# Kernel optimization log

Hardware: AMD Instinct MI355X
Metric: run time of the kernel (lower is better)

The kernel has to match this reference:

```python
import jax, jax.numpy as jnp
import numpy as np

M = 8192        # tokens (batch*seq)
K = 14336       # d_ff (input features of down proj)
N = 4096        # d_model (output features)
GROUP = 128     # quantization group size along K


def unpack_int4(w_packed):
    """[N, K//8] int32 -> [N, K] signed int4 values in [-8, 7] (float32)."""
    n, kp = w_packed.shape
    shifts = (jnp.arange(8, dtype=jnp.int32) * 4)  # nibble 0 = lowest bits
    nib = (w_packed[:, :, None] >> shifts) & 0xF   # [N, K//8, 8]
    nib = nib - jnp.where(nib >= 8, 16, 0)         # sign-extend 4-bit
    return nib.reshape(n, kp * 8).astype(jnp.float32)


def setup_inputs() -> dict:
    key = jax.random.key(0)
    ks = jax.random.split(key, 6)
    qx = jax.random.normal(ks[0], (M, K), dtype=jnp.float32)
    qxscale = jax.random.uniform(ks[1], (M, 1), dtype=jnp.float32) * 0.05 + 0.001
    residual = jax.random.normal(ks[2], (M, N), dtype=jnp.float32)
    weight_i4 = jax.random.randint(ks[3], (N, K // 8), jnp.iinfo(jnp.int32).min,
                                   jnp.iinfo(jnp.int32).max, dtype=jnp.int32)
    weight_scale = jax.random.uniform(ks[4], (N, K // GROUP), dtype=jnp.float32) * 0.02 + 0.001
    bias = jax.random.normal(ks[5], (N,), dtype=jnp.float32)
    return {"qx": qx, "qxscale": qxscale, "residual": residual,
            "weight_i4": weight_i4, "weight_scale": weight_scale,
            "bias": bias, "group_size": GROUP}


def reference(qx, qxscale, residual, weight_i4, weight_scale, bias, group_size):
    # 1) unpack int32 -> signed int4
    iw = unpack_int4(weight_i4)                          # [N, K]
    n, k = iw.shape
    g = k // group_size
    # 2) group-wise dequantize (one scale per group along K, per output row)
    dq = (iw.reshape(n, g, group_size) * weight_scale[:, :, None]).reshape(n, k)
    # 3) matmul x @ W^T, 4) per-token scale, residual + bias
    y = jnp.einsum('mk,nk->mn', qx, dq) * qxscale + residual + bias
    return y
```

## Files before the change

### kernel.cpp

```cpp
#include <hip/hip_runtime.h>
#include <hip/hip_bf16.h>
#include <stdint.h>

#define M_DIM 8192
#define K_DIM 14336
#define N_DIM 4096
#define GROUP_SZ 128
#define NGROUP (K_DIM / GROUP_SZ)

typedef short short8 __attribute__((ext_vector_type(8)));
typedef float f32x4 __attribute__((ext_vector_type(4)));
typedef int i32x4 __attribute__((ext_vector_type(4)));

static __device__ __forceinline__ short f2bf(float f) {
  unsigned u = __builtin_bit_cast(unsigned, f);
  u += 0x7FFFu + ((u >> 16) & 1u);
  return (short)(u >> 16);
}

static __device__ __forceinline__ void gload_lds16(const void* g, void* lds) {
  __builtin_amdgcn_global_load_lds(
      (const __attribute__((address_space(1))) unsigned int*)g,
      (__attribute__((address_space(3))) unsigned int*)lds, 16, 0, 0);
}


__global__ __launch_bounds__(256) void dp_quant_x(const float* __restrict__ x,
                                                  char* __restrict__ xq,
                                                  float* __restrict__ sx) {
  __shared__ float rowbuf[K_DIM];
  __shared__ float red[256];
  const int row = blockIdx.x;
  const int t = threadIdx.x;
  const float* xr = x + (size_t)row * K_DIM;
  float amax = 0.f;
#pragma unroll
  for (int j = 0; j < 14; ++j) {
    float4 v = *(const float4*)(xr + j * 1024 + t * 4);
    *(float4*)(rowbuf + j * 1024 + t * 4) = v;
    amax = fmaxf(amax,
                 fmaxf(fmaxf(fabsf(v.x), fabsf(v.y)), fmaxf(fabsf(v.z), fabsf(v.w))));
  }
  red[t] = amax;
  __syncthreads();
  for (int s = 128; s > 0; s >>= 1) {
    if (t < s) red[t] = fmaxf(red[t], red[t + s]);
    __syncthreads();
  }
  const float am = red[0];
  const float inv = (am > 0.f) ? 127.f / am : 0.f;
  if (t == 0) sx[row] = am * (1.f / 127.f);
  char* xo = xq + (size_t)row * K_DIM;
#pragma unroll
  for (int j = 0; j < 14; ++j) {
    float4 v = *(const float4*)(rowbuf + j * 1024 + t * 4);
    char4 q;
    q.x = (char)__float2int_rn(v.x * inv);
    q.y = (char)__float2int_rn(v.y * inv);
    q.z = (char)__float2int_rn(v.z * inv);
    q.w = (char)__float2int_rn(v.w * inv);
    *(char4*)(xo + j * 1024 + t * 4) = q;
  }
}

__global__ __launch_bounds__(256) void dp_repack_w(const int* __restrict__ wq,
                                                   const float* __restrict__ wsc,
                                                   char* __restrict__ w8,
                                                   float* __restrict__ sw) {
  __shared__ float wsl[NGROUP];
  const int n = blockIdx.x;
  const int t = threadIdx.x;
  if (t < NGROUP) wsl[t] = wsc[(size_t)n * NGROUP + t];
  __syncthreads();
  float mx = 0.f;
#pragma unroll
  for (int g = 0; g < NGROUP; ++g) mx = fmaxf(mx, wsl[g]);
  const float invsw = 15.875f / mx;
  if (t == 0) sw[n] = mx * (8.f / 127.f);
#pragma unroll
  for (int j = 0; j < 7; ++j) {
    int p = t + 256 * j;
    int w = wq[(size_t)n * (K_DIM / 8) + p];
    float sc = wsl[p >> 4] * invsw;
    unsigned lo = 0, hi = 0;
#pragma unroll
    for (int b = 0; b < 4; ++b) {
      int q = (w << (28 - 4 * b)) >> 28;
      int r = __float2int_rn((float)q * sc);
      lo |= (unsigned)(r & 0xff) << (8 * b);
    }
#pragma unroll
    for (int b = 4; b < 8; ++b) {
      int q = (w << (28 - 4 * b)) >> 28;
      int r = __float2int_rn((float)q * sc);
      hi |= (unsigned)(r & 0xff) << (8 * (b - 4));
    }
    *(uint2*)(w8 + (size_t)n * K_DIM + (size_t)p * 8) = make_uint2(lo, hi);
  }
}

__global__ __launch_bounds__(512, 2) void dp_gemm8i(
    const char* __restrict__ Xq, const char* __restrict__ Wq8,
    const float* __restrict__ sw, const float* __restrict__ sx,
    const float* __restrict__ qxscale, const float* __restrict__ residual,
    const float* __restrict__ bias, float* __restrict__ out) {
  __shared__ __align__(16) char lds[65536];

  const int tid = threadIdx.x;
  const int lane = tid & 63;
  const int wid = tid >> 6;
  const int wm = wid >> 2, wn = wid & 3;
  const int lr = lane & 15, lg = lane >> 4;

  const int wg = blockIdx.x;
  const int swz = (wg & 7) * 64 + (wg >> 3);
  const int m0 = (swz >> 4) * 256;
  const int n0 = (swz & 15) * 256;

  const int slot = (lg ^ ((lr >> 1) & 3)) << 4;
  int offA[2][4], offB[2][2];
#pragma unroll
  for (int mh = 0; mh < 2; ++mh)
#pragma unroll
    for (int mf = 0; mf < 4; ++mf)
      offA[mh][mf] = (mh * 128 + wm * 64 + mf * 16 + lr) * 64 + slot;
#pragma unroll
  for (int nh = 0; nh < 2; ++nh)
#pragma unroll
    for (int nf = 0; nf < 2; ++nf)
      offB[nh][nf] = (nh * 128 + wn * 32 + nf * 16 + lr) * 64 + slot;

  const int srow = tid >> 2;
  const int ksrc = ((tid & 3) ^ ((tid >> 3) & 3)) * 16;
  const size_t aRow = (size_t)(m0 + srow) * K_DIM + ksrc;
  const size_t bRow = (size_t)(n0 + srow) * K_DIM + ksrc;
  const int dst0 = tid * 16;

  i32x4 acc[8][4];
#pragma unroll
  for (int i = 0; i < 8; ++i)
#pragma unroll
    for (int j = 0; j < 4; ++j) acc[i][j] = (i32x4){0, 0, 0, 0};

  i32x4 aF[4];
  i32x4 bF[2][2];

#define STAGE_A(kt, h)                                                         \
  gload_lds16(Xq + aRow + (size_t)((h) * 128) * K_DIM + (size_t)(kt) * 64,     \
              lds + (((kt) & 1) << 14) + ((h) << 13) + dst0)
#define STAGE_B(kt, h)                                                         \
  gload_lds16(Wq8 + bRow + (size_t)((h) * 128) * K_DIM + (size_t)(kt) * 64,    \
              lds + 32768 + (((kt) & 1) << 14) + ((h) << 13) + dst0)
#define FENCE asm volatile("" ::: "memory")

#define PHASE(kt, mh, nh, LA, LB, STMT, WMT)                                   \
  do {                                                                         \
    if (LA) {                                                                  \
      const char* Ab_ = lds + (((kt) & 1) << 14);                              \
      _Pragma("unroll") for (int mf = 0; mf < 4; ++mf)                         \
          aF[mf] = *(const i32x4*)(Ab_ + offA[mh][mf]);                        \
    }                                                                          \
    if (LB) {                                                                  \
      const char* Bb_ = lds + 32768 + (((kt) & 1) << 14);                      \
      _Pragma("unroll") for (int nf = 0; nf < 2; ++nf)                         \
          bF[nh][nf] = *(const i32x4*)(Bb_ + offB[nh][nf]);                    \
    }                                                                          \
    STMT;                                                                      \
    FENCE;                                                                     \
    WMT;                                                                       \
    __builtin_amdgcn_s_barrier();                                              \
    FENCE;                                                                     \
    __builtin_amdgcn_s_setprio(1);                                             \
    _Pragma("unroll") for (int mf = 0; mf < 4; ++mf)                           \
        _Pragma("unroll") for (int nf = 0; nf < 2; ++nf)                       \
            acc[(mh) * 4 + mf][(nh) * 2 + nf] =                                \
                __builtin_amdgcn_mfma_i32_16x16x64_i8(                         \
                    aF[mf], bF[nh][nf], acc[(mh) * 4 + mf][(nh) * 2 + nf],     \
                    0, 0, 0);                                                  \
    __builtin_amdgcn_s_setprio(0);                                             \
    FENCE;                                                                     \
  } while (0)

  STAGE_A(0, 0); STAGE_A(0, 1); STAGE_B(0, 0); STAGE_B(0, 1);
  STAGE_A(1, 0); STAGE_B(1, 0);
  FENCE;
  asm volatile("s_waitcnt vmcnt(2)" ::: "memory");
  __builtin_amdgcn_s_barrier();
  FENCE;

  for (int i = 0; i < 112; ++i) {
    const int t = 2 * i;
    const bool st = (i < 111);
    PHASE(t, 0, 0, 1, 1, { STAGE_A(t + 1, 1); }, {});
    PHASE(t, 0, 1, 0, 1, { STAGE_B(t + 1, 1); }, {});
    PHASE(t, 1, 0, 1, 0, { if (st) STAGE_A(t + 2, 0); }, {});
    PHASE(t, 1, 1, 0, 0, { if (st) STAGE_B(t + 2, 0); },
          {
            if (st) asm volatile("s_waitcnt vmcnt(2)" ::: "memory");
            else    asm volatile("s_waitcnt vmcnt(0)" ::: "memory");
          });
    PHASE(t + 1, 0, 0, 1, 1, { if (st) STAGE_A(t + 2, 1); }, {});
    PHASE(t + 1, 0, 1, 0, 1, { if (st) STAGE_B(t + 2, 1); }, {});
    PHASE(t + 1, 1, 0, 1, 0, { if (st) STAGE_A(t + 3, 0); }, {});
    PHASE(t + 1, 1, 1, 0, 0, { if (st) STAGE_B(t + 3, 0); },
          {
            if (st) asm volatile("s_waitcnt vmcnt(2)" ::: "memory");
            else    asm volatile("s_waitcnt vmcnt(0)" ::: "memory");
          });
  }

#pragma unroll
  for (int mh = 0; mh < 2; ++mh)
#pragma unroll
    for (int mf = 0; mf < 4; ++mf)
#pragma unroll
      for (int nh = 0; nh < 2; ++nh)
#pragma unroll
        for (int nf = 0; nf < 2; ++nf) {
          int n = n0 + nh * 128 + wn * 32 + nf * 16 + lr;
          float bv = bias[n];
          float swn = sw[n];
          i32x4 v = acc[mh * 4 + mf][nh * 2 + nf];
#pragma unroll
          for (int rr = 0; rr < 4; ++rr) {
            int m = m0 + mh * 128 + wm * 64 + mf * 16 + lg * 4 + rr;
            size_t off = (size_t)m * N_DIM + n;
            out[off] = (float)v[rr] * (qxscale[m] * sx[m] * swn) + residual[off] + bv;
          }
        }
#undef PHASE
#undef STAGE_A
#undef STAGE_B
#undef FENCE
}


__global__ __launch_bounds__(256) void dp_dequant_w(const int* __restrict__ wq,
                                                    const float* __restrict__ wsc,
                                                    short* __restrict__ wb) {
  int p = blockIdx.x * 256 + threadIdx.x;
  int n = blockIdx.y;
  int w = wq[(size_t)n * (K_DIM / 8) + p];
  float sc = wsc[(size_t)n * NGROUP + (p >> 4)];
  short8 v;
#pragma unroll
  for (int j = 0; j < 8; ++j) {
    int q = (w << (28 - 4 * j)) >> 28;
    v[j] = f2bf((float)q * sc);
  }
  *(short8*)(wb + (size_t)n * K_DIM + (size_t)p * 8) = v;
}

template <int BMODE>
__global__ __launch_bounds__(256) void dp_gemm(
    const float* __restrict__ qx, const int* __restrict__ Wq,
    const float* __restrict__ Wsc, const short* __restrict__ Wb,
    const float* __restrict__ qxscale, const float* __restrict__ residual,
    const float* __restrict__ bias, float* __restrict__ out) {
  __shared__ short As[128 * 64];
  __shared__ short Bs[128 * 64];

  const int tid = threadIdx.x;
  const int lane = tid & 63;
  const int w = tid >> 6;

  const int nwg = gridDim.x;
  const int cpx = nwg >> 3;
  const int wg = blockIdx.x;
  const int swz = (wg & 7) * cpx + (wg >> 3);
  const int bm = swz / (N_DIM / 128);
  const int bn = swz % (N_DIM / 128);
  const int m0 = bm * 128, n0 = bn * 128;

  const int wm = w >> 1, wn = w & 1;
  const int lr = lane & 15, lg = lane >> 4;

  f32x4 acc[4][4];
#pragma unroll
  for (int i = 0; i < 4; ++i)
#pragma unroll
    for (int j = 0; j < 4; ++j) acc[i][j] = (f32x4){0.f, 0.f, 0.f, 0.f};

  for (int kt = 0; kt < K_DIM / 64; ++kt) {
    const int k0 = kt * 64;
#pragma unroll
    for (int i = 0; i < 4; ++i) {
      int ldsb = i * 4096 + tid * 16;
      int row = ldsb >> 7;
      int slog = ((ldsb >> 4) & 7) ^ (row & 7);
      const float4* p = (const float4*)(qx + (size_t)(m0 + row) * K_DIM + k0 + slog * 8);
      float4 u0 = p[0], u1 = p[1];
      short8 v;
      v[0] = f2bf(u0.x); v[1] = f2bf(u0.y); v[2] = f2bf(u0.z); v[3] = f2bf(u0.w);
      v[4] = f2bf(u1.x); v[5] = f2bf(u1.y); v[6] = f2bf(u1.z); v[7] = f2bf(u1.w);
      *(short8*)((char*)As + ldsb) = v;
    }
    if (BMODE == 0) {
#pragma unroll
      for (int i = 0; i < 4; ++i) {
        int ldsb = i * 4096 + w * 1024 + lane * 16;
        int row = ldsb >> 7;
        int slog = ((ldsb >> 4) & 7) ^ (row & 7);
        gload_lds16(Wb + (size_t)(n0 + row) * K_DIM + k0 + slog * 8, (char*)Bs + ldsb);
      }
    } else {
      int row = tid >> 1;
      int kb = (tid & 1) * 32;
      int4 pw = *(const int4*)(Wq + (size_t)(n0 + row) * (K_DIM / 8) + (k0 + kb) / 8);
      float sc = Wsc[(size_t)(n0 + row) * NGROUP + (k0 + kb) / GROUP_SZ];
      int pv[4] = {pw.x, pw.y, pw.z, pw.w};
#pragma unroll
      for (int p = 0; p < 4; ++p) {
        short8 v;
#pragma unroll
        for (int j = 0; j < 8; ++j) {
          int q = (pv[p] << (28 - 4 * j)) >> 28;
          v[j] = f2bf((float)q * sc);
        }
        int slog = (tid & 1) * 4 + p;
        int sp = slog ^ (row & 7);
        *(short8*)((char*)Bs + row * 128 + sp * 16) = v;
      }
    }
    __syncthreads();
#pragma unroll
    for (int s = 0; s < 2; ++s) {
      short8 a[4], b[4];
#pragma unroll
      for (int f = 0; f < 4; ++f) {
        int row = wm * 64 + f * 16 + lr;
        int sp = (s * 4 + lg) ^ (row & 7);
        a[f] = *(const short8*)((char*)As + row * 128 + sp * 16);
      }
#pragma unroll
      for (int f = 0; f < 4; ++f) {
        int row = wn * 64 + f * 16 + lr;
        int sp = (s * 4 + lg) ^ (row & 7);
        b[f] = *(const short8*)((char*)Bs + row * 128 + sp * 16);
      }
#pragma unroll
      for (int i = 0; i < 4; ++i)
#pragma unroll
        for (int j = 0; j < 4; ++j)
          acc[i][j] = __builtin_amdgcn_mfma_f32_16x16x32_bf16(a[i], b[j], acc[i][j], 0, 0, 0);
    }
    __syncthreads();
  }

  const int mb = m0 + wm * 64, nb = n0 + wn * 64;
#pragma unroll
  for (int i = 0; i < 4; ++i)
#pragma unroll
    for (int j = 0; j < 4; ++j) {
      int n = nb + j * 16 + lr;
      float bv = bias[n];
#pragma unroll
      for (int r = 0; r < 4; ++r) {
        int m = mb + i * 16 + lg * 4 + r;
        size_t off = (size_t)m * N_DIM + n;
        out[off] = acc[i][j][r] * qxscale[m] + residual[off] + bv;
      }
    }
}

extern "C" void kernel_launch(void* const* d_in, const int* in_sizes, int n_in,
                              void* d_out, int out_size, void* d_ws, size_t ws_size,
                              hipStream_t stream) {
  const float* qx = (const float*)d_in[0];
  const float* qxscale = (const float*)d_in[1];
  const float* residual = (const float*)d_in[2];
  const int* wq = (const int*)d_in[3];
  const float* wsc = (const float*)d_in[4];
  const float* bias = (const float*)d_in[5];
  float* out = (float*)d_out;

  const size_t SZ_W8 = (size_t)N_DIM * K_DIM;
  const size_t SZ_XQ = (size_t)M_DIM * K_DIM;
  const size_t OFF_XQ = SZ_W8;
  const size_t OFF_SW = OFF_XQ + SZ_XQ;
  const size_t OFF_SX = OFF_SW + (size_t)N_DIM * 4;
  const size_t need_i8 = OFF_SX + (size_t)M_DIM * 4;
  const size_t need_w = (size_t)N_DIM * K_DIM * 2;

  if (ws_size >= need_i8) {
    char* w8 = (char*)d_ws;
    char* xq = (char*)d_ws + OFF_XQ;
    float* sw = (float*)((char*)d_ws + OFF_SW);
    float* sx = (float*)((char*)d_ws + OFF_SX);
    dp_repack_w<<<dim3(N_DIM), dim3(256), 0, stream>>>(wq, wsc, w8, sw);
    dp_quant_x<<<dim3(M_DIM), dim3(256), 0, stream>>>(qx, xq, sx);
    dp_gemm8i<<<dim3((M_DIM / 256) * (N_DIM / 256)), dim3(512), 0, stream>>>(
        xq, w8, sw, sx, qxscale, residual, bias, out);
  } else if (ws_size >= need_w) {
    short* wb = (short*)d_ws;
    dp_dequant_w<<<dim3(K_DIM / 8 / 256, N_DIM), dim3(256), 0, stream>>>(wq, wsc, wb);
    dp_gemm<0><<<dim3(2048), dim3(256), 0, stream>>>(qx, wq, wsc, wb, qxscale,
                                                     residual, bias, out);
  } else {
    dp_gemm<1><<<dim3(2048), dim3(256), 0, stream>>>(qx, wq, wsc, nullptr, qxscale,
                                                     residual, bias, out);
  }
}
```

Baseline: 579.2 us.

## Double the K tile to 128 with 128KB LDS and an 8-way swizzle

Result: faster. 506.1 us, median of 3 (-12.6%).

```diff
diff --git a/kernel.cpp b/kernel.cpp
--- a/kernel.cpp
+++ b/kernel.cpp
@@ -104,7 +104,7 @@
     const float* __restrict__ sw, const float* __restrict__ sx,
     const float* __restrict__ qxscale, const float* __restrict__ residual,
     const float* __restrict__ bias, float* __restrict__ out) {
-  __shared__ __align__(16) char lds[65536];
+  __shared__ __align__(16) char lds[131072];
 
   const int tid = threadIdx.x;
   const int lane = tid & 63;
@@ -117,21 +117,24 @@
   const int m0 = (swz >> 4) * 256;
   const int n0 = (swz & 15) * 256;
 
-  const int slot = (lg ^ ((lr >> 1) & 3)) << 4;
-  int offA[2][4], offB[2][2];
-#pragma unroll
-  for (int mh = 0; mh < 2; ++mh)
-#pragma unroll
-    for (int mf = 0; mf < 4; ++mf)
-      offA[mh][mf] = (mh * 128 + wm * 64 + mf * 16 + lr) * 64 + slot;
-#pragma unroll
-  for (int nh = 0; nh < 2; ++nh)
-#pragma unroll
-    for (int nf = 0; nf < 2; ++nf)
-      offB[nh][nf] = (nh * 128 + wn * 32 + nf * 16 + lr) * 64 + slot;
-
-  const int srow = tid >> 2;
-  const int ksrc = ((tid & 3) ^ ((tid >> 3) & 3)) * 16;
+  int offA[4][2], offB[2][2];
+#pragma unroll
+  for (int mf = 0; mf < 4; ++mf) {
+    int r = wm * 64 + mf * 16 + lr;
+#pragma unroll
+    for (int kk = 0; kk < 2; ++kk)
+      offA[mf][kk] = r * 128 + (((kk * 4 + lg) ^ (r & 7)) << 4);
+  }
+#pragma unroll
+  for (int nf = 0; nf < 2; ++nf) {
+    int r = wn * 32 + nf * 16 + lr;
+#pragma unroll
+    for (int kk = 0; kk < 2; ++kk)
+      offB[nf][kk] = r * 128 + (((kk * 4 + lg) ^ (r & 7)) << 4);
+  }
+
+  const int srow = tid >> 3;
+  const int ksrc = ((tid & 7) ^ (srow & 7)) * 16;
   const size_t aRow = (size_t)(m0 + srow) * K_DIM + ksrc;
   const size_t bRow = (size_t)(n0 + srow) * K_DIM + ksrc;
   const int dst0 = tid * 16;
@@ -142,28 +145,40 @@
 #pragma unroll
     for (int j = 0; j < 4; ++j) acc[i][j] = (i32x4){0, 0, 0, 0};
 
-  i32x4 aF[4];
-  i32x4 bF[2][2];
-
-#define STAGE_A(kt, h)                                                         \
-  gload_lds16(Xq + aRow + (size_t)((h) * 128) * K_DIM + (size_t)(kt) * 64,     \
-              lds + (((kt) & 1) << 14) + ((h) << 13) + dst0)
-#define STAGE_B(kt, h)                                                         \
-  gload_lds16(Wq8 + bRow + (size_t)((h) * 128) * K_DIM + (size_t)(kt) * 64,    \
-              lds + 32768 + (((kt) & 1) << 14) + ((h) << 13) + dst0)
+  i32x4 aF[4][2];
+  i32x4 bF[2][2][2];
+
+#define STAGE_A(T, h)                                                          \
+  do {                                                                         \
+    size_t g_ = aRow + (size_t)((h) * 128) * K_DIM + (size_t)(T) * 128;        \
+    int d_ = (((T) & 1) << 15) + ((h) << 14) + dst0;                           \
+    gload_lds16(Xq + g_, lds + d_);                                            \
+    gload_lds16(Xq + g_ + (size_t)64 * K_DIM, lds + d_ + 8192);                \
+  } while (0)
+
+#define STAGE_B(T, h)                                                          \
+  do {                                                                         \
+    size_t g_ = bRow + (size_t)((h) * 128) * K_DIM + (size_t)(T) * 128;        \
+    int d_ = 65536 + (((T) & 1) << 15) + ((h) << 14) + dst0;                   \
+    gload_lds16(Wq8 + g_, lds + d_);                                           \
+    gload_lds16(Wq8 + g_ + (size_t)64 * K_DIM, lds + d_ + 8192);               \
+  } while (0)
+
 #define FENCE asm volatile("" ::: "memory")
 
-#define PHASE(kt, mh, nh, LA, LB, STMT, WMT)                                   \
+#define PHASE(T, mh, nh, LA, LB, STMT, WMT)                                    \
   do {                                                                         \
     if (LA) {                                                                  \
-      const char* Ab_ = lds + (((kt) & 1) << 14);                              \
+      const char* Ab_ = lds + ((((T) & 1) << 15) + ((mh) << 14));              \
       _Pragma("unroll") for (int mf = 0; mf < 4; ++mf)                         \
-          aF[mf] = *(const i32x4*)(Ab_ + offA[mh][mf]);                        \
+          _Pragma("unroll") for (int kk = 0; kk < 2; ++kk)                     \
+              aF[mf][kk] = *(const i32x4*)(Ab_ + offA[mf][kk]);                \
     }                                                                          \
     if (LB) {                                                                  \
-      const char* Bb_ = lds + 32768 + (((kt) & 1) << 14);                      \
+      const char* Bb_ = lds + (65536 + (((T) & 1) << 15) + ((nh) << 14));      \
       _Pragma("unroll") for (int nf = 0; nf < 2; ++nf)                         \
-          bF[nh][nf] = *(const i32x4*)(Bb_ + offB[nh][nf]);                    \
+          _Pragma("unroll") for (int kk = 0; kk < 2; ++kk)                     \
+              bF[nh][nf][kk] = *(const i32x4*)(Bb_ + offB[nf][kk]);            \
     }                                                                          \
     STMT;                                                                      \
     FENCE;                                                                     \
@@ -171,32 +186,33 @@
     __builtin_amdgcn_s_barrier();                                              \
     FENCE;                                                                     \
     __builtin_amdgcn_s_setprio(1);                                             \
-    _Pragma("unroll") for (int mf = 0; mf < 4; ++mf)                           \
-        _Pragma("unroll") for (int nf = 0; nf < 2; ++nf)                       \
-            acc[(mh) * 4 + mf][(nh) * 2 + nf] =                                \
-                __builtin_amdgcn_mfma_i32_16x16x64_i8(                         \
-                    aF[mf], bF[nh][nf], acc[(mh) * 4 + mf][(nh) * 2 + nf],     \
-                    0, 0, 0);                                                  \
+    _Pragma("unroll") for (int kk = 0; kk < 2; ++kk)                           \
+        _Pragma("unroll") for (int mf = 0; mf < 4; ++mf)                       \
+            _Pragma("unroll") for (int nf = 0; nf < 2; ++nf)                   \
+                acc[(mh) * 4 + mf][(nh) * 2 + nf] =                            \
+                    __builtin_amdgcn_mfma_i32_16x16x64_i8(                     \
+                        aF[mf][kk], bF[nh][nf][kk],                            \
+                        acc[(mh) * 4 + mf][(nh) * 2 + nf], 0, 0, 0);           \
     __builtin_amdgcn_s_setprio(0);                                             \
     FENCE;                                                                     \
   } while (0)
 
-  STAGE_A(0, 0); STAGE_A(0, 1); STAGE_B(0, 0); STAGE_B(0, 1);
+  STAGE_A(0, 0); STAGE_B(0, 0); STAGE_A(0, 1); STAGE_B(0, 1);
   STAGE_A(1, 0); STAGE_B(1, 0);
   FENCE;
-  asm volatile("s_waitcnt vmcnt(2)" ::: "memory");
+  asm volatile("s_waitcnt vmcnt(4)" ::: "memory");
   __builtin_amdgcn_s_barrier();
   FENCE;
 
-  for (int i = 0; i < 112; ++i) {
+  for (int i = 0; i < 56; ++i) {
     const int t = 2 * i;
-    const bool st = (i < 111);
+    const bool st = (i < 55);
     PHASE(t, 0, 0, 1, 1, { STAGE_A(t + 1, 1); }, {});
     PHASE(t, 0, 1, 0, 1, { STAGE_B(t + 1, 1); }, {});
     PHASE(t, 1, 0, 1, 0, { if (st) STAGE_A(t + 2, 0); }, {});
     PHASE(t, 1, 1, 0, 0, { if (st) STAGE_B(t + 2, 0); },
           {
-            if (st) asm volatile("s_waitcnt vmcnt(2)" ::: "memory");
+            if (st) asm volatile("s_waitcnt vmcnt(4)" ::: "memory");
             else    asm volatile("s_waitcnt vmcnt(0)" ::: "memory");
           });
     PHASE(t + 1, 0, 0, 1, 1, { if (st) STAGE_A(t + 2, 1); }, {});
@@ -204,7 +220,7 @@
     PHASE(t + 1, 1, 0, 1, 0, { if (st) STAGE_A(t + 3, 0); }, {});
     PHASE(t + 1, 1, 1, 0, 0, { if (st) STAGE_B(t + 3, 0); },
           {
-            if (st) asm volatile("s_waitcnt vmcnt(2)" ::: "memory");
+            if (st) asm volatile("s_waitcnt vmcnt(4)" ::: "memory");
             else    asm volatile("s_waitcnt vmcnt(0)" ::: "memory");
           });
   }
```

## Shrink int8 GEMM tile to 256x128 with triple-buffered LDS pipeline

Applied to the files above, without the earlier changes.

New measurement: 679.6 us. 1.17x slower.

```diff
diff --git a/kernel.cpp b/kernel.cpp
--- a/kernel.cpp
+++ b/kernel.cpp
@@ -99,138 +99,105 @@
   }
 }
 
-__global__ __launch_bounds__(512, 2) void dp_gemm8i(
+__global__ __launch_bounds__(512, 4) void dp_gemm8i(
     const char* __restrict__ Xq, const char* __restrict__ Wq8,
     const float* __restrict__ sw, const float* __restrict__ sx,
     const float* __restrict__ qxscale, const float* __restrict__ residual,
     const float* __restrict__ bias, float* __restrict__ out) {
-  __shared__ __align__(16) char lds[65536];
+  __shared__ __align__(16) char lds[73728];
 
   const int tid = threadIdx.x;
   const int lane = tid & 63;
   const int wid = tid >> 6;
-  const int wm = wid >> 2, wn = wid & 3;
+  const int wm = wid >> 1, wn = wid & 1;
   const int lr = lane & 15, lg = lane >> 4;
 
   const int wg = blockIdx.x;
-  const int swz = (wg & 7) * 64 + (wg >> 3);
-  const int m0 = (swz >> 4) * 256;
-  const int n0 = (swz & 15) * 256;
-
-  const int slot = (lg ^ ((lr >> 1) & 3)) << 4;
-  int offA[2][4], offB[2][2];
-#pragma unroll
-  for (int mh = 0; mh < 2; ++mh)
-#pragma unroll
-    for (int mf = 0; mf < 4; ++mf)
-      offA[mh][mf] = (mh * 128 + wm * 64 + mf * 16 + lr) * 64 + slot;
-#pragma unroll
-  for (int nh = 0; nh < 2; ++nh)
-#pragma unroll
-    for (int nf = 0; nf < 2; ++nf)
-      offB[nh][nf] = (nh * 128 + wn * 32 + nf * 16 + lr) * 64 + slot;
+  const int swz = (wg & 7) * 128 + (wg >> 3);
+  const int m0 = (swz >> 5) * 256;
+  const int n0 = (swz & 31) * 128;
+
+  const int slot16 = (lg ^ ((lr >> 1) & 3)) << 4;
+  int offA[4], offB[4];
+#pragma unroll
+  for (int mf = 0; mf < 4; ++mf)
+    offA[mf] = (wm * 64 + mf * 16 + lr) * 64 + slot16;
+#pragma unroll
+  for (int nf = 0; nf < 4; ++nf)
+    offB[nf] = (wn * 64 + nf * 16 + lr) * 64 + slot16;
 
   const int srow = tid >> 2;
-  const int ksrc = ((tid & 3) ^ ((tid >> 3) & 3)) * 16;
-  const size_t aRow = (size_t)(m0 + srow) * K_DIM + ksrc;
-  const size_t bRow = (size_t)(n0 + srow) * K_DIM + ksrc;
+  const int ksrc = ((tid & 3) ^ ((srow >> 1) & 3)) * 16;
+  const char* gA = Xq + (size_t)(m0 + srow) * K_DIM + ksrc;
+  const char* gB = Wq8 + (size_t)(n0 + srow) * K_DIM + ksrc;
   const int dst0 = tid * 16;
 
-  i32x4 acc[8][4];
-#pragma unroll
-  for (int i = 0; i < 8; ++i)
+  char *a0 = lds, *a1 = lds + 16384, *a2 = lds + 32768;
+  char *b0 = lds + 49152, *b1 = lds + 57344, *b2 = lds + 65536;
+
+  i32x4 acc[4][4];
+#pragma unroll
+  for (int i = 0; i < 4; ++i)
 #pragma unroll
     for (int j = 0; j < 4; ++j) acc[i][j] = (i32x4){0, 0, 0, 0};
 
-  i32x4 aF[4];
-  i32x4 bF[2][2];
-
-#define STAGE_A(kt, h)                                                         \
-  gload_lds16(Xq + aRow + (size_t)((h) * 128) * K_DIM + (size_t)(kt) * 64,     \
-              lds + (((kt) & 1) << 14) + ((h) << 13) + dst0)
-#define STAGE_B(kt, h)                                                         \
-  gload_lds16(Wq8 + bRow + (size_t)((h) * 128) * K_DIM + (size_t)(kt) * 64,    \
-              lds + 32768 + (((kt) & 1) << 14) + ((h) << 13) + dst0)
+#define STAGE(kb, pa, pb)                                                      \
+  do {                                                                         \
+    gload_lds16(gA + (size_t)(kb), (pa) + dst0);                               \
+    gload_lds16(gA + (size_t)(kb) + (size_t)128 * K_DIM, (pa) + 8192 + dst0);  \
+    gload_lds16(gB + (size_t)(kb), (pb) + dst0);                               \
+  } while (0)
+
 #define FENCE asm volatile("" ::: "memory")
 
-#define PHASE(kt, mh, nh, LA, LB, STMT, WMT)                                   \
-  do {                                                                         \
-    if (LA) {                                                                  \
-      const char* Ab_ = lds + (((kt) & 1) << 14);                              \
-      _Pragma("unroll") for (int mf = 0; mf < 4; ++mf)                         \
-          aF[mf] = *(const i32x4*)(Ab_ + offA[mh][mf]);                        \
-    }                                                                          \
-    if (LB) {                                                                  \
-      const char* Bb_ = lds + 32768 + (((kt) & 1) << 14);                      \
-      _Pragma("unroll") for (int nf = 0; nf < 2; ++nf)                         \
-          bF[nh][nf] = *(const i32x4*)(Bb_ + offB[nh][nf]);                    \
-    }                                                                          \
-    STMT;                                                                      \
-    FENCE;                                                                     \
-    WMT;                                                                       \
-    __builtin_amdgcn_s_barrier();                                              \
-    FENCE;                                                                     \
-    __builtin_amdgcn_s_setprio(1);                                             \
-    _Pragma("unroll") for (int mf = 0; mf < 4; ++mf)                           \
-        _Pragma("unroll") for (int nf = 0; nf < 2; ++nf)                       \
-            acc[(mh) * 4 + mf][(nh) * 2 + nf] =                                \
-                __builtin_amdgcn_mfma_i32_16x16x64_i8(                         \
-                    aF[mf], bF[nh][nf], acc[(mh) * 4 + mf][(nh) * 2 + nf],     \
-                    0, 0, 0);                                                  \
-    __builtin_amdgcn_s_setprio(0);                                             \
-    FENCE;                                                                     \
-  } while (0)
-
-  STAGE_A(0, 0); STAGE_A(0, 1); STAGE_B(0, 0); STAGE_B(0, 1);
-  STAGE_A(1, 0); STAGE_B(1, 0);
+  STAGE(0, a0, b0);
+  STAGE(64, a1, b1);
   FENCE;
-  asm volatile("s_waitcnt vmcnt(2)" ::: "memory");
+  asm volatile("s_waitcnt vmcnt(3)" ::: "memory");
   __builtin_amdgcn_s_barrier();
   FENCE;
 
-  for (int i = 0; i < 112; ++i) {
-    const int t = 2 * i;
-    const bool st = (i < 111);
-    PHASE(t, 0, 0, 1, 1, { STAGE_A(t + 1, 1); }, {});
-    PHASE(t, 0, 1, 0, 1, { STAGE_B(t + 1, 1); }, {});
-    PHASE(t, 1, 0, 1, 0, { if (st) STAGE_A(t + 2, 0); }, {});
-    PHASE(t, 1, 1, 0, 0, { if (st) STAGE_B(t + 2, 0); },
-          {
-            if (st) asm volatile("s_waitcnt vmcnt(2)" ::: "memory");
-            else    asm volatile("s_waitcnt vmcnt(0)" ::: "memory");
-          });
-    PHASE(t + 1, 0, 0, 1, 1, { if (st) STAGE_A(t + 2, 1); }, {});
-    PHASE(t + 1, 0, 1, 0, 1, { if (st) STAGE_B(t + 2, 1); }, {});
-    PHASE(t + 1, 1, 0, 1, 0, { if (st) STAGE_A(t + 3, 0); }, {});
-    PHASE(t + 1, 1, 1, 0, 0, { if (st) STAGE_B(t + 3, 0); },
-          {
-            if (st) asm volatile("s_waitcnt vmcnt(2)" ::: "memory");
-            else    asm volatile("s_waitcnt vmcnt(0)" ::: "memory");
-          });
-  }
-
-#pragma unroll
-  for (int mh = 0; mh < 2; ++mh)
+  for (int T = 0; T < 224; ++T) {
+    i32x4 aF[4], bF[4];
+#pragma unroll
+    for (int mf = 0; mf < 4; ++mf) aF[mf] = *(const i32x4*)(a0 + offA[mf]);
+#pragma unroll
+    for (int nf = 0; nf < 4; ++nf) bF[nf] = *(const i32x4*)(b0 + offB[nf]);
+    if (T < 222) STAGE((size_t)(T + 2) * 64, a2, b2);
+    FENCE;
+    if (T < 222) asm volatile("s_waitcnt vmcnt(3)" ::: "memory");
+    else         asm volatile("s_waitcnt vmcnt(0)" ::: "memory");
+    __builtin_amdgcn_s_barrier();
+    FENCE;
+    __builtin_amdgcn_s_setprio(1);
 #pragma unroll
     for (int mf = 0; mf < 4; ++mf)
 #pragma unroll
-      for (int nh = 0; nh < 2; ++nh)
-#pragma unroll
-        for (int nf = 0; nf < 2; ++nf) {
-          int n = n0 + nh * 128 + wn * 32 + nf * 16 + lr;
-          float bv = bias[n];
-          float swn = sw[n];
-          i32x4 v = acc[mh * 4 + mf][nh * 2 + nf];
-#pragma unroll
-          for (int rr = 0; rr < 4; ++rr) {
-            int m = m0 + mh * 128 + wm * 64 + mf * 16 + lg * 4 + rr;
-            size_t off = (size_t)m * N_DIM + n;
-            out[off] = (float)v[rr] * (qxscale[m] * sx[m] * swn) + residual[off] + bv;
-          }
-        }
-#undef PHASE
-#undef STAGE_A
-#undef STAGE_B
+      for (int nf = 0; nf < 4; ++nf)
+        acc[mf][nf] = __builtin_amdgcn_mfma_i32_16x16x64_i8(aF[mf], bF[nf],
+                                                            acc[mf][nf], 0, 0, 0);
+    __builtin_amdgcn_s_setprio(0);
+    FENCE;
+    char* t0 = a0; a0 = a1; a1 = a2; a2 = t0;
+    char* t1 = b0; b0 = b1; b1 = b2; b2 = t1;
+  }
+
+#pragma unroll
+  for (int mf = 0; mf < 4; ++mf)
+#pragma unroll
+    for (int nf = 0; nf < 4; ++nf) {
+      int n = n0 + wn * 64 + nf * 16 + lr;
+      float bv = bias[n];
+      float swn = sw[n];
+      i32x4 v = acc[mf][nf];
+#pragma unroll
+      for (int rr = 0; rr < 4; ++rr) {
+        int m = m0 + wm * 64 + mf * 16 + lg * 4 + rr;
+        size_t off = (size_t)m * N_DIM + n;
+        out[off] = (float)v[rr] * (qxscale[m] * sx[m] * swn) + residual[off] + bv;
+      }
+    }
+#undef STAGE
 #undef FENCE
 }
 
@@ -389,7 +356,7 @@
     float* sx = (float*)((char*)d_ws + OFF_SX);
     dp_repack_w<<<dim3(N_DIM), dim3(256), 0, stream>>>(wq, wsc, w8, sw);
     dp_quant_x<<<dim3(M_DIM), dim3(256), 0, stream>>>(qx, xq, sx);
-    dp_gemm8i<<<dim3((M_DIM / 256) * (N_DIM / 256)), dim3(512), 0, stream>>>(
+    dp_gemm8i<<<dim3((M_DIM / 256) * (N_DIM / 128)), dim3(512), 0, stream>>>(
         xq, w8, sw, sx, qxscale, residual, bias, out);
   } else if (ws_size >= need_w) {
     short* wb = (short*)d_ws;
```
